# Optimization experiments

Measured on AMD Instinct MI355X. Metric: run time of the kernel, lower is better.

Reference implementation:

```python
import jax, jax.numpy as jnp
import numpy as np

RADIUS = 0.15   # group_args['radius']
NSAMPLE = 32    # group_args['nsample']
EPS = 1e-5      # BatchNorm eps


def ball_query(p, radius, k):
    # p: [B,N,3]; returns neighbor indices [B,N,K] (first K points within radius,
    # padded with the first hit -- PointNet++ ball-query semantics; self is always a hit)
    N = p.shape[1]
    d2 = jnp.sum((p[:, :, None, :] - p[:, None, :, :]) ** 2, axis=-1)  # [B,N,N]
    idx = jnp.where(d2 < radius * radius,
                    jnp.arange(N, dtype=jnp.int32)[None, None, :], N)
    idx = jnp.sort(idx, axis=-1)[..., :k]
    return jnp.where(idx == N, idx[..., :1], idx)


def conv_bn_relu(x, W, gamma, beta, mean, var):
    # 1x1 conv2d (pointwise over [N,K]) + eval-mode BN2d + ReLU
    x = jnp.einsum('oc,bcnk->bonk', W, x)
    scale = (gamma / jnp.sqrt(var + EPS))[None, :, None, None]
    shift = (beta - mean * gamma / jnp.sqrt(var + EPS))[None, :, None, None]
    return jax.nn.relu(x * scale + shift)


def setup_inputs() -> dict:
    key = jax.random.key(0)
    ks = jax.random.split(key, 4)
    B, N, C = 2, 8192, 64
    C1, C2 = 128, 128
    Cin = C + 3  # CHANNEL_MAP['dp_fj']
    return {
        'p': jax.random.uniform(ks[0], (B, N, 3), jnp.float32),
        'f': jax.random.normal(ks[1], (B, C, N), jnp.float32),
        'W1': jax.random.normal(ks[2], (C1, Cin), jnp.float32) / np.float32(np.sqrt(Cin)),
        'gamma1': jnp.ones((C1,), jnp.float32),
        'beta1': jnp.zeros((C1,), jnp.float32),
        'mean1': jnp.zeros((C1,), jnp.float32),
        'var1': jnp.ones((C1,), jnp.float32),
        'W2': jax.random.normal(ks[3], (C2, C1), jnp.float32) / np.float32(np.sqrt(C1)),
        'gamma2': jnp.ones((C2,), jnp.float32),
        'beta2': jnp.zeros((C2,), jnp.float32),
        'mean2': jnp.zeros((C2,), jnp.float32),
        'var2': jnp.ones((C2,), jnp.float32),
    }


def reference(p, f, W1, gamma1, beta1, mean1, var1, W2, gamma2, beta2, mean2, var2):
    # p: [B,N,3], f: [B,C,N]
    idx = ball_query(p, RADIUS, NSAMPLE)                                   # [B,N,K]
    gp = jnp.take_along_axis(p[:, None, :, :], idx[:, :, :, None], axis=2)  # [B,N,K,3]
    dp = jnp.transpose(gp - p[:, :, None, :], (0, 3, 1, 2))                 # [B,3,N,K]
    fj = jnp.take_along_axis(f[:, :, None, :], idx[:, None, :, :], axis=3)  # [B,C,N,K]
    x = jnp.concatenate([dp, fj], axis=1)                                   # dp_fj: [B,3+C,N,K]
    x = conv_bn_relu(x, W1, gamma1, beta1, mean1, var1)
    x = conv_bn_relu(x, W2, gamma2, beta2, mean2, var2)
    return jnp.max(x, axis=-1)                                              # [B,C2,N]
```

## Files before the change

### kernel.cpp

```cpp
#include <hip/hip_runtime.h>
#include <math.h>

#define NSAMPLE 32
constexpr int B_ = 2, N_ = 8192, C_ = 64, C1_ = 128, C2_ = 128, CIN_ = 67;
constexpr int KP = 96;
constexpr int XPAD = 104;
constexpr int HPAD = 136;
constexpr float BQ_R2 = 0.15f * 0.15f;
constexpr float EPS_ = 1e-5f;
constexpr int NCELL = 216;

typedef __attribute__((ext_vector_type(8))) short bf16x8;
typedef __attribute__((ext_vector_type(4))) short short4v;
typedef __attribute__((ext_vector_type(4))) float f32x4;
typedef unsigned long long ull;

__device__ __forceinline__ short f2bf(float x) {
    union { float f; unsigned u; } v; v.f = x;
    return (short)((v.u + 0x7FFFu + ((v.u >> 16) & 1u)) >> 16);
}
__device__ __forceinline__ int cell_id(float x, float y, float z) {
    int cx = min((int)(x * 6.0f), 5);
    int cy = min((int)(y * 6.0f), 5);
    int cz = min((int)(z * 6.0f), 5);
    return (cz * 6 + cy) * 6 + cx;
}

constexpr int TBLK = (B_ * N_) / 256;
constexpr int CBLK0 = TBLK + 1;

__global__ __launch_bounds__(256) void prep_kernel(
    const float* __restrict__ p, const float* __restrict__ f,
    short* __restrict__ fT, int* __restrict__ counts,
    const float* __restrict__ W1,
    const float* __restrict__ g1, const float* __restrict__ b1,
    const float* __restrict__ m1, const float* __restrict__ v1,
    const float* __restrict__ W2,
    const float* __restrict__ g2, const float* __restrict__ b2,
    const float* __restrict__ m2, const float* __restrict__ v2,
    short* __restrict__ W1p, short* __restrict__ W2p, float* __restrict__ bn)
{
    int blk = blockIdx.x;
    if (blk < TBLK) {
        int g = blk * 256 + threadIdx.x;
        int b = g >> 13, n = g & (N_ - 1);
        const float* fb = f + (size_t)b * C_ * N_ + n;
        short* row = fT + (size_t)g * C_;
        #pragma unroll
        for (int c0 = 0; c0 < C_; c0 += 8) {
            bf16x8 v;
            #pragma unroll
            for (int c = 0; c < 8; ++c) v[c] = f2bf(fb[(size_t)(c0 + c) * N_]);
            *(bf16x8*)&row[c0] = v;
        }
    } else if (blk == TBLK) {
        if (threadIdx.x >= 128) return;
        int t = threadIdx.x;
        short* r1 = W1p + t * KP;
        #pragma unroll
        for (int k = 0; k < 3; ++k) r1[k] = f2bf(W1[t * CIN_ + k]);
        #pragma unroll
        for (int k = 3; k < 8; ++k) r1[k] = 0;
        for (int c = 0; c < 64; ++c) r1[8 + c] = f2bf(W1[t * CIN_ + 3 + c]);
        #pragma unroll
        for (int k = 72; k < KP; ++k) r1[k] = 0;
        short* r2 = W2p + t * C1_;
        for (int c = 0; c < C1_; ++c) r2[c] = f2bf(W2[t * C1_ + c]);
        float s1 = g1[t] * rsqrtf(v1[t] + EPS_);
        bn[t] = s1;            bn[128 + t] = b1[t] - m1[t] * s1;
        float s2 = g2[t] * rsqrtf(v2[t] + EPS_);
        bn[256 + t] = s2;      bn[384 + t] = b2[t] - m2[t] * s2;
    } else {
        int g = (blk - CBLK0) * 256 + threadIdx.x;
        int b = g >> 13, n = g & (N_ - 1);
        const float* q = p + (size_t)b * N_ * 3 + 3 * n;
        int c = cell_id(q[0], q[1], q[2]);
        atomicAdd(&counts[b * 256 + c], 1);
    }
}

__global__ __launch_bounds__(128) void prefix_kernel(
    const int* __restrict__ counts, int* __restrict__ starts)
{
    int w = threadIdx.x >> 6, lane = threadIdx.x & 63;
    const int* cnt = counts + w * 256;
    int* st = starts + w * 256;
    int off = 0;
    #pragma unroll
    for (int ch = 0; ch < 4; ++ch) {
        int i = ch * 64 + lane;
        int v = (i < NCELL) ? cnt[i] : 0;
        int incl = v;
        #pragma unroll
        for (int d = 1; d < 64; d <<= 1) {
            int t = __shfl_up(incl, d, 64);
            if (lane >= d) incl += t;
        }
        if (i <= NCELL) st[i] = off + incl - v;
        off += __shfl(incl, 63, 64);
    }
}

__global__ __launch_bounds__(256) void scatter_kernel(
    const float* __restrict__ p, const int* __restrict__ starts,
    int* __restrict__ cursors, int* __restrict__ lists)
{
    int g = blockIdx.x * 256 + threadIdx.x;
    int b = g >> 13, n = g & (N_ - 1);
    const float* q = p + (size_t)b * N_ * 3 + 3 * n;
    int c = cell_id(q[0], q[1], q[2]);
    int slot = starts[b * 256 + c] + atomicAdd(&cursors[b * 256 + c], 1);
    lists[(b << 13) + slot] = n;
}

__global__ __launch_bounds__(256) void grid_query_kernel(
    const float* __restrict__ p, const int* __restrict__ starts,
    const int* __restrict__ lists, int* __restrict__ idx)
{
    __shared__ ull bitmap[4][128];
    int tid = threadIdx.x, lane = tid & 63, w = tid >> 6;
    int wid = blockIdx.x * 4 + w;
    int b = wid >> 13, n = wid & (N_ - 1);
    const float* pb = p + (size_t)b * N_ * 3;
    const int* st = starts + b * 256;
    const int* ls = lists + (b << 13);
    float qx = pb[3 * n], qy = pb[3 * n + 1], qz = pb[3 * n + 2];

    #pragma unroll
    for (int i = lane; i < 128; i += 64) bitmap[w][i] = 0;

    int cx = min((int)(qx * 6.0f), 5);
    int cy = min((int)(qy * 6.0f), 5);
    int cz = min((int)(qz * 6.0f), 5);
    int x0 = max(cx - 1, 0), x1 = min(cx + 1, 5);

    int segBase[9], segLen[9], total = 0;
    #pragma unroll
    for (int s = 0; s < 9; ++s) {
        int zz = cz - 1 + s / 3, yy = cy - 1 + s % 3;
        bool ok = (zz >= 0 && zz < 6 && yy >= 0 && yy < 6);
        int zc = min(max(zz, 0), 5), yc = min(max(yy, 0), 5);
        int row = (zc * 6 + yc) * 6;
        int s0 = st[row + x0], s1 = st[row + x1 + 1];
        segBase[s] = s0;
        segLen[s] = ok ? (s1 - s0) : 0;
        total += segLen[s];
    }

    for (int o0 = 0; o0 < total; o0 += 64) {
        int o = o0 + lane;
        if (o < total) {
            int rem = o, addr = -1;
            #pragma unroll
            for (int s = 0; s < 9; ++s) {
                if (rem >= 0 && rem < segLen[s] && addr < 0) addr = segBase[s] + rem;
                rem -= segLen[s];
            }
            int j = ls[addr];
            float dx = __fadd_rn(pb[3 * j],     -qx);
            float dy = __fadd_rn(pb[3 * j + 1], -qy);
            float dz = __fadd_rn(pb[3 * j + 2], -qz);
            float d2 = __fadd_rn(__fadd_rn(__fmul_rn(dx, dx), __fmul_rn(dy, dy)),
                                 __fmul_rn(dz, dz));
            if (d2 < BQ_R2)
                atomicOr(&bitmap[w][j >> 6], 1ull << (j & 63));
        }
    }
    __threadfence_block();

    ull w0 = bitmap[w][2 * lane], w1 = bitmap[w][2 * lane + 1];
    int c = __popcll(w0) + __popcll(w1);
    int incl = c;
    #pragma unroll
    for (int d = 1; d < 64; d <<= 1) {
        int t = __shfl_up(incl, d, 64);
        if (lane >= d) incl += t;
    }
    int pref = incl - c;
    int total_hits = __shfl(incl, 63, 64);
    int* out = idx + (size_t)wid * NSAMPLE;

    int rank = pref;
    ull ww = w0;
    int basebit = lane * 128;
    while (ww && rank < NSAMPLE) {
        int bpos = __builtin_ctzll(ww);
        out[rank] = basebit + bpos;
        ++rank; ww &= ww - 1;
    }
    ww = w1; basebit += 64;
    while (ww && rank < NSAMPLE) {
        int bpos = __builtin_ctzll(ww);
        out[rank] = basebit + bpos;
        ++rank; ww &= ww - 1;
    }

    if (total_hits < NSAMPLE) {
        ull m = __ballot(c > 0);
        int l0 = __ffsll((long long)m) - 1;
        int fb_local = w0 ? __builtin_ctzll(w0) : 64 + __builtin_ctzll(w1);
        int first = __shfl(fb_local, l0, 64) + l0 * 128;
        for (int k2 = total_hits + lane; k2 < NSAMPLE; k2 += 64) out[k2] = first;
    }
}

__global__ __launch_bounds__(256) void fused_mfma_kernel(
    const float* __restrict__ p, const int* __restrict__ idx,
    const short* __restrict__ fT, const short* __restrict__ W1p,
    const short* __restrict__ W2p, const float* __restrict__ bn,
    float* __restrict__ out)
{
    __shared__ short smem[128 * HPAD];
    __shared__ float sBN[4][128];
    __shared__ int sidx[128];

    int tid = threadIdx.x;
    int bk = blockIdx.x;
    bk = (bk & 7) * 512 + (bk >> 3);
    int b = bk >> 11;
    int n0 = (bk & 2047) * 4;
    int lane = tid & 63, w = tid >> 6;
    int lr = lane & 15, lq = lane >> 4;

    if (tid < 128) {
        sBN[0][tid] = bn[tid];       sBN[1][tid] = bn[128 + tid];
        sBN[2][tid] = bn[256 + tid]; sBN[3][tid] = bn[384 + tid];
        sidx[tid] = idx[((size_t)((b << 13) + n0)) * NSAMPLE + tid];
    }
    __syncthreads();

    const float* pb = p + (size_t)b * N_ * 3;
    #pragma unroll
    for (int pass = 0; pass < 4; ++pass) {
        int col = pass * 32 + (tid >> 3);
        int part = tid & 7;
        int j = sidx[col];
        *(bf16x8*)&smem[col * XPAD + 8 + part * 8] =
            *(const bf16x8*)&fT[((size_t)(b << 13) + j) * C_ + part * 8];
        if (part == 0) {
            int n = n0 + (col >> 5);
            bf16x8 v = {0, 0, 0, 0, 0, 0, 0, 0};
            v[0] = f2bf(__fadd_rn(pb[3 * j],     -pb[3 * n]));
            v[1] = f2bf(__fadd_rn(pb[3 * j + 1], -pb[3 * n + 1]));
            v[2] = f2bf(__fadd_rn(pb[3 * j + 2], -pb[3 * n + 2]));
            *(bf16x8*)&smem[col * XPAD] = v;
        } else if (part <= 3) {
            bf16x8 z = {0, 0, 0, 0, 0, 0, 0, 0};
            *(bf16x8*)&smem[col * XPAD + 72 + (part - 1) * 8] = z;
        }
    }
    __syncthreads();

    int wr = (w & 1) * 64;
    int wc = (w >> 1) * 64;

    f32x4 acc[4][4];
    #pragma unroll
    for (int m = 0; m < 4; ++m)
        #pragma unroll
        for (int nt = 0; nt < 4; ++nt) acc[m][nt] = (f32x4){0.f, 0.f, 0.f, 0.f};
    #pragma unroll
    for (int ks = 0; ks < 3; ++ks) {
        bf16x8 a[4];
        #pragma unroll
        for (int m = 0; m < 4; ++m)
            a[m] = *(const bf16x8*)&W1p[(wr + m * 16 + lr) * KP + ks * 32 + lq * 8];
        #pragma unroll
        for (int nt = 0; nt < 4; ++nt) {
            bf16x8 bf = *(const bf16x8*)&smem[(wc + nt * 16 + lr) * XPAD + ks * 32 + lq * 8];
            #pragma unroll
            for (int m = 0; m < 4; ++m)
                acc[m][nt] = __builtin_amdgcn_mfma_f32_16x16x32_bf16(a[m], bf, acc[m][nt], 0, 0, 0);
        }
    }
    __syncthreads();

    #pragma unroll
    for (int m = 0; m < 4; ++m) {
        int rb = wr + m * 16 + lq * 4;
        float s0 = sBN[0][rb], s1 = sBN[0][rb + 1], s2 = sBN[0][rb + 2], s3 = sBN[0][rb + 3];
        float h0 = sBN[1][rb], h1 = sBN[1][rb + 1], h2 = sBN[1][rb + 2], h3 = sBN[1][rb + 3];
        #pragma unroll
        for (int nt = 0; nt < 4; ++nt) {
            int col = wc + nt * 16 + lr;
            short4v hv;
            hv[0] = f2bf(fmaxf(fmaf(acc[m][nt][0], s0, h0), 0.f));
            hv[1] = f2bf(fmaxf(fmaf(acc[m][nt][1], s1, h1), 0.f));
            hv[2] = f2bf(fmaxf(fmaf(acc[m][nt][2], s2, h2), 0.f));
            hv[3] = f2bf(fmaxf(fmaf(acc[m][nt][3], s3, h3), 0.f));
            *(short4v*)&smem[col * HPAD + rb] = hv;
        }
    }
    __syncthreads();

    f32x4 acc2[4][4];
    #pragma unroll
    for (int m = 0; m < 4; ++m)
        #pragma unroll
        for (int nt = 0; nt < 4; ++nt) acc2[m][nt] = (f32x4){0.f, 0.f, 0.f, 0.f};
    #pragma unroll
    for (int ks = 0; ks < 4; ++ks) {
        bf16x8 a[4];
        #pragma unroll
        for (int m = 0; m < 4; ++m)
            a[m] = *(const bf16x8*)&W2p[(wr + m * 16 + lr) * C1_ + ks * 32 + lq * 8];
        #pragma unroll
        for (int nt = 0; nt < 4; ++nt) {
            bf16x8 bf = *(const bf16x8*)&smem[(wc + nt * 16 + lr) * HPAD + ks * 32 + lq * 8];
            #pragma unroll
            for (int m = 0; m < 4; ++m)
                acc2[m][nt] = __builtin_amdgcn_mfma_f32_16x16x32_bf16(a[m], bf, acc2[m][nt], 0, 0, 0);
        }
    }

    #pragma unroll
    for (int m = 0; m < 4; ++m) {
        int rb = wr + m * 16 + lq * 4;
        float s0 = sBN[2][rb], s1 = sBN[2][rb + 1], s2 = sBN[2][rb + 2], s3 = sBN[2][rb + 3];
        float h0 = sBN[3][rb], h1 = sBN[3][rb + 1], h2 = sBN[3][rb + 2], h3 = sBN[3][rb + 3];
        #pragma unroll
        for (int lp = 0; lp < 2; ++lp) {
            int n = n0 + (w >> 1) * 2 + lp;
            float v0 = fmaxf(fmaf(acc2[m][2 * lp][0], s0, h0), fmaf(acc2[m][2 * lp + 1][0], s0, h0));
            float v1 = fmaxf(fmaf(acc2[m][2 * lp][1], s1, h1), fmaf(acc2[m][2 * lp + 1][1], s1, h1));
            float v2 = fmaxf(fmaf(acc2[m][2 * lp][2], s2, h2), fmaf(acc2[m][2 * lp + 1][2], s2, h2));
            float v3 = fmaxf(fmaf(acc2[m][2 * lp][3], s3, h3), fmaf(acc2[m][2 * lp + 1][3], s3, h3));
            #pragma unroll
            for (int st = 1; st <= 8; st <<= 1) {
                v0 = fmaxf(v0, __shfl_xor(v0, st, 64));
                v1 = fmaxf(v1, __shfl_xor(v1, st, 64));
                v2 = fmaxf(v2, __shfl_xor(v2, st, 64));
                v3 = fmaxf(v3, __shfl_xor(v3, st, 64));
            }
            if (lr == 0) {
                out[((size_t)(b * C2_ + rb))     * N_ + n] = fmaxf(v0, 0.f);
                out[((size_t)(b * C2_ + rb + 1)) * N_ + n] = fmaxf(v1, 0.f);
                out[((size_t)(b * C2_ + rb + 2)) * N_ + n] = fmaxf(v2, 0.f);
                out[((size_t)(b * C2_ + rb + 3)) * N_ + n] = fmaxf(v3, 0.f);
            }
        }
    }
}

extern "C" void kernel_launch(void* const* d_in, const int* in_sizes, int n_in,
                              void* d_out, int out_size, void* d_ws, size_t ws_size,
                              hipStream_t stream) {
    const float* p   = (const float*)d_in[0];
    const float* f   = (const float*)d_in[1];
    const float* W1  = (const float*)d_in[2];
    const float* g1  = (const float*)d_in[3];
    const float* bb1 = (const float*)d_in[4];
    const float* m1  = (const float*)d_in[5];
    const float* v1  = (const float*)d_in[6];
    const float* W2  = (const float*)d_in[7];
    const float* g2  = (const float*)d_in[8];
    const float* bb2 = (const float*)d_in[9];
    const float* m2  = (const float*)d_in[10];
    const float* v2  = (const float*)d_in[11];
    float* out = (float*)d_out;

    char* ws = (char*)d_ws;
    int*   idxbuf = (int*)ws;
    short* fT  = (short*)(ws + (2 << 20));
    short* W1p = (short*)(ws + (4 << 20));
    short* W2p = (short*)(ws + (4 << 20) + 0x6000);
    float* bnv = (float*)(ws + (4 << 20) + 0xE000);
    char*  gm  = ws + (4 << 20) + 0x10000;
    int* counts  = (int*)gm;
    int* cursors = (int*)(gm + 0x800);
    int* starts  = (int*)(gm + 0x1000);
    int* lists   = (int*)(gm + 0x2000);

    hipMemsetAsync(gm, 0, 0x1000, stream);
    prep_kernel<<<CBLK0 + 64, 256, 0, stream>>>(
        p, f, fT, counts, W1, g1, bb1, m1, v1, W2, g2, bb2, m2, v2,
        W1p, W2p, bnv);
    prefix_kernel<<<1, 128, 0, stream>>>(counts, starts);
    scatter_kernel<<<64, 256, 0, stream>>>(p, starts, cursors, lists);
    grid_query_kernel<<<(B_ * N_) / 4, 256, 0, stream>>>(p, starts, lists, idxbuf);
    fused_mfma_kernel<<<(B_ * N_) / 4, 256, 0, stream>>>(
        p, idxbuf, fT, W1p, W2p, bnv, out);
}
```

Before: 217.8 us.

## Precompute per-point layer-1 feature GEMM and fuse ball query into MLP kernel

Splits the first conv so the feature part (W1·f with BN scale) is computed once per point in a separate MFMA GEMM, stored as bf16 Y. Per-neighbor work then gathers Y rows and adds the 3-channel relative-position term with scalar FMAs. This removes the K-fold redundant layer-1 GEMM. The grid ball query is also merged into the MLP kernel, which drops the global idx buffer and one launch. The cost is an extra bf16 rounding of the pre-activation Y, plus a transposed layer-2 MFMA layout.

```diff
diff --git a/kernel.cpp b/kernel.cpp
--- a/kernel.cpp
+++ b/kernel.cpp
@@ -3,12 +3,8 @@
 
 #define NSAMPLE 32
 constexpr int B_ = 2, N_ = 8192, C_ = 64, C1_ = 128, C2_ = 128, CIN_ = 67;
-constexpr int KP = 96;
-constexpr int XPAD = 104;
-constexpr int HPAD = 136;
 constexpr float BQ_R2 = 0.15f * 0.15f;
 constexpr float EPS_ = 1e-5f;
-constexpr int NCELL = 216;
 
 typedef __attribute__((ext_vector_type(8))) short bf16x8;
 typedef __attribute__((ext_vector_type(4))) short short4v;
@@ -18,6 +14,10 @@
 __device__ __forceinline__ short f2bf(float x) {
     union { float f; unsigned u; } v; v.f = x;
     return (short)((v.u + 0x7FFFu + ((v.u >> 16) & 1u)) >> 16);
+}
+__device__ __forceinline__ float bf2f(short s) {
+    union { float f; unsigned u; } v; v.u = ((unsigned)(unsigned short)s) << 16;
+    return v.f;
 }
 __device__ __forceinline__ int cell_id(float x, float y, float z) {
     int cx = min((int)(x * 6.0f), 5);
@@ -27,7 +27,6 @@
 }
 
 constexpr int TBLK = (B_ * N_) / 256;
-constexpr int CBLK0 = TBLK + 1;
 
 __global__ __launch_bounds__(256) void prep_kernel(
     const float* __restrict__ p, const float* __restrict__ f,
@@ -38,7 +37,8 @@
     const float* __restrict__ W2,
     const float* __restrict__ g2, const float* __restrict__ b2,
     const float* __restrict__ m2, const float* __restrict__ v2,
-    short* __restrict__ W1p, short* __restrict__ W2p, float* __restrict__ bn)
+    short* __restrict__ W1fp, short* __restrict__ W2p,
+    float* __restrict__ Wd, float* __restrict__ bn)
 {
     int blk = blockIdx.x;
     if (blk < TBLK) {
@@ -56,22 +56,19 @@
     } else if (blk == TBLK) {
         if (threadIdx.x >= 128) return;
         int t = threadIdx.x;
-        short* r1 = W1p + t * KP;
-        #pragma unroll
-        for (int k = 0; k < 3; ++k) r1[k] = f2bf(W1[t * CIN_ + k]);
-        #pragma unroll
-        for (int k = 3; k < 8; ++k) r1[k] = 0;
-        for (int c = 0; c < 64; ++c) r1[8 + c] = f2bf(W1[t * CIN_ + 3 + c]);
-        #pragma unroll
-        for (int k = 72; k < KP; ++k) r1[k] = 0;
+        float s1 = g1[t] * rsqrtf(v1[t] + EPS_);
+        float s2 = g2[t] * rsqrtf(v2[t] + EPS_);
+        bn[t] = s1;            bn[128 + t] = b1[t] - m1[t] * s1;
+        bn[256 + t] = s2;      bn[384 + t] = b2[t] - m2[t] * s2;
+        Wd[t]       = s1 * W1[t * CIN_ + 0];
+        Wd[128 + t] = s1 * W1[t * CIN_ + 1];
+        Wd[256 + t] = s1 * W1[t * CIN_ + 2];
+        short* r1 = W1fp + t * 64;
+        for (int c = 0; c < 64; ++c) r1[c] = f2bf(W1[t * CIN_ + 3 + c]);
         short* r2 = W2p + t * C1_;
         for (int c = 0; c < C1_; ++c) r2[c] = f2bf(W2[t * C1_ + c]);
-        float s1 = g1[t] * rsqrtf(v1[t] + EPS_);
-        bn[t] = s1;            bn[128 + t] = b1[t] - m1[t] * s1;
-        float s2 = g2[t] * rsqrtf(v2[t] + EPS_);
-        bn[256 + t] = s2;      bn[384 + t] = b2[t] - m2[t] * s2;
     } else {
-        int g = (blk - CBLK0) * 256 + threadIdx.x;
+        int g = (blk - TBLK - 1) * 256 + threadIdx.x;
         int b = g >> 13, n = g & (N_ - 1);
         const float* q = p + (size_t)b * N_ * 3 + 3 * n;
         int c = cell_id(q[0], q[1], q[2]);
@@ -89,210 +86,200 @@
     #pragma unroll
     for (int ch = 0; ch < 4; ++ch) {
         int i = ch * 64 + lane;
-        int v = (i < NCELL) ? cnt[i] : 0;
+        int v = (i < 216) ? cnt[i] : 0;
         int incl = v;
         #pragma unroll
         for (int d = 1; d < 64; d <<= 1) {
             int t = __shfl_up(incl, d, 64);
             if (lane >= d) incl += t;
         }
-        if (i <= NCELL) st[i] = off + incl - v;
+        if (i <= 216) st[i] = off + incl - v;
         off += __shfl(incl, 63, 64);
     }
 }
 
-__global__ __launch_bounds__(256) void scatter_kernel(
+__global__ __launch_bounds__(256) void scatter_ygemm_kernel(
     const float* __restrict__ p, const int* __restrict__ starts,
-    int* __restrict__ cursors, int* __restrict__ lists)
+    int* __restrict__ cursors, int* __restrict__ lists,
+    const short* __restrict__ fT, const short* __restrict__ W1fp,
+    const float* __restrict__ bn, short* __restrict__ Y)
 {
-    int g = blockIdx.x * 256 + threadIdx.x;
-    int b = g >> 13, n = g & (N_ - 1);
-    const float* q = p + (size_t)b * N_ * 3 + 3 * n;
-    int c = cell_id(q[0], q[1], q[2]);
-    int slot = starts[b * 256 + c] + atomicAdd(&cursors[b * 256 + c], 1);
-    lists[(b << 13) + slot] = n;
-}
-
-__global__ __launch_bounds__(256) void grid_query_kernel(
+    int blk = blockIdx.x;
+    if (blk < 64) {
+        int g = blk * 256 + threadIdx.x;
+        int b = g >> 13, n = g & (N_ - 1);
+        const float* q = p + (size_t)b * N_ * 3 + 3 * n;
+        int c = cell_id(q[0], q[1], q[2]);
+        int slot = starts[b * 256 + c] + atomicAdd(&cursors[b * 256 + c], 1);
+        lists[(b << 13) + slot] = n;
+        return;
+    }
+    int q = blk - 64;
+    int gs0 = q * 128;
+    int tid = threadIdx.x, lane = tid & 63, w = tid >> 6;
+    int lr = lane & 15, lq = lane >> 4;
+    int rq = (w & 1) * 64, cq = (w >> 1) * 64;
+    f32x4 acc[4][4];
+    #pragma unroll
+    for (int m = 0; m < 4; ++m)
+        #pragma unroll
+        for (int nt = 0; nt < 4; ++nt) acc[m][nt] = (f32x4){0.f, 0.f, 0.f, 0.f};
+    #pragma unroll
+    for (int ks = 0; ks < 2; ++ks) {
+        bf16x8 a[4];
+        #pragma unroll
+        for (int m = 0; m < 4; ++m)
+            a[m] = *(const bf16x8*)&W1fp[(rq + m * 16 + lr) * 64 + ks * 32 + lq * 8];
+        #pragma unroll
+        for (int nt = 0; nt < 4; ++nt) {
+            bf16x8 bfr = *(const bf16x8*)&fT[((size_t)(gs0 + cq + nt * 16 + lr)) * 64 + ks * 32 + lq * 8];
+            #pragma unroll
+            for (int m = 0; m < 4; ++m)
+                acc[m][nt] = __builtin_amdgcn_mfma_f32_16x16x32_bf16(a[m], bfr, acc[m][nt], 0, 0, 0);
+        }
+    }
+    #pragma unroll
+    for (int m = 0; m < 4; ++m) {
+        int rb = rq + m * 16 + lq * 4;
+        f32x4 sc = *(const f32x4*)&bn[rb];
+        f32x4 sh = *(const f32x4*)&bn[128 + rb];
+        #pragma unroll
+        for (int nt = 0; nt < 4; ++nt) {
+            int gs = gs0 + cq + nt * 16 + lr;
+            short4v yv;
+            yv[0] = f2bf(fmaf(acc[m][nt][0], sc[0], sh[0]));
+            yv[1] = f2bf(fmaf(acc[m][nt][1], sc[1], sh[1]));
+            yv[2] = f2bf(fmaf(acc[m][nt][2], sc[2], sh[2]));
+            yv[3] = f2bf(fmaf(acc[m][nt][3], sc[3], sh[3]));
+            *(short4v*)&Y[(size_t)gs * 128 + rb] = yv;
+        }
+    }
+}
+
+__global__ __launch_bounds__(256) void fused_kernel(
     const float* __restrict__ p, const int* __restrict__ starts,
-    const int* __restrict__ lists, int* __restrict__ idx)
+    const int* __restrict__ lists, const short* __restrict__ Y,
+    const short* __restrict__ W2p, const float* __restrict__ Wd,
+    const float* __restrict__ bn, float* __restrict__ out)
 {
     __shared__ ull bitmap[4][128];
-    int tid = threadIdx.x, lane = tid & 63, w = tid >> 6;
-    int wid = blockIdx.x * 4 + w;
-    int b = wid >> 13, n = wid & (N_ - 1);
+    __shared__ int sidx[4][NSAMPLE];
+    __shared__ short HT[16 * 128 * 8];
+
+    int tid = threadIdx.x;
+    int bk = blockIdx.x;
+    bk = (bk & 7) * 512 + (bk >> 3);
+    int b = bk >> 11, n0 = (bk & 2047) * 4;
+    int lane = tid & 63, w = tid >> 6;
+    int lr = lane & 15, lq = lane >> 4;
     const float* pb = p + (size_t)b * N_ * 3;
     const int* st = starts + b * 256;
     const int* ls = lists + (b << 13);
-    float qx = pb[3 * n], qy = pb[3 * n + 1], qz = pb[3 * n + 2];
-
-    #pragma unroll
-    for (int i = lane; i < 128; i += 64) bitmap[w][i] = 0;
-
+
+    int nq = n0 + w;
+    float qx = pb[3 * nq], qy = pb[3 * nq + 1], qz = pb[3 * nq + 2];
+    *(f32x4*)&bitmap[w][2 * lane] = (f32x4){0.f, 0.f, 0.f, 0.f};
     int cx = min((int)(qx * 6.0f), 5);
     int cy = min((int)(qy * 6.0f), 5);
     int cz = min((int)(qz * 6.0f), 5);
     int x0 = max(cx - 1, 0), x1 = min(cx + 1, 5);
-
-    int segBase[9], segLen[9], total = 0;
-    #pragma unroll
-    for (int s = 0; s < 9; ++s) {
-        int zz = cz - 1 + s / 3, yy = cy - 1 + s % 3;
-        bool ok = (zz >= 0 && zz < 6 && yy >= 0 && yy < 6);
-        int zc = min(max(zz, 0), 5), yc = min(max(yy, 0), 5);
-        int row = (zc * 6 + yc) * 6;
-        int s0 = st[row + x0], s1 = st[row + x1 + 1];
-        segBase[s] = s0;
-        segLen[s] = ok ? (s1 - s0) : 0;
-        total += segLen[s];
-    }
-
-    for (int o0 = 0; o0 < total; o0 += 64) {
-        int o = o0 + lane;
-        if (o < total) {
-            int rem = o, addr = -1;
-            #pragma unroll
-            for (int s = 0; s < 9; ++s) {
-                if (rem >= 0 && rem < segLen[s] && addr < 0) addr = segBase[s] + rem;
-                rem -= segLen[s];
+    for (int s9 = 0; s9 < 9; ++s9) {
+        int zz = cz - 1 + s9 / 3, yy = cy - 1 + s9 % 3;
+        if (zz < 0 || zz > 5 || yy < 0 || yy > 5) continue;
+        int row = (zz * 6 + yy) * 6;
+        int s0 = st[row + x0];
+        int len = st[row + x1 + 1] - s0;
+        for (int o0 = 0; o0 < len; o0 += 64) {
+            int o = o0 + lane;
+            if (o < len) {
+                int j = ls[s0 + o];
+                float dx = __fadd_rn(pb[3 * j],     -qx);
+                float dy = __fadd_rn(pb[3 * j + 1], -qy);
+                float dz = __fadd_rn(pb[3 * j + 2], -qz);
+                float d2 = __fadd_rn(__fadd_rn(__fmul_rn(dx, dx), __fmul_rn(dy, dy)),
+                                     __fmul_rn(dz, dz));
+                if (d2 < BQ_R2)
+                    atomicOr(&bitmap[w][j >> 6], 1ull << (j & 63));
             }
-            int j = ls[addr];
-            float dx = __fadd_rn(pb[3 * j],     -qx);
-            float dy = __fadd_rn(pb[3 * j + 1], -qy);
-            float dz = __fadd_rn(pb[3 * j + 2], -qz);
-            float d2 = __fadd_rn(__fadd_rn(__fmul_rn(dx, dx), __fmul_rn(dy, dy)),
-                                 __fmul_rn(dz, dz));
-            if (d2 < BQ_R2)
-                atomicOr(&bitmap[w][j >> 6], 1ull << (j & 63));
-        }
-    }
-    __threadfence_block();
-
-    ull w0 = bitmap[w][2 * lane], w1 = bitmap[w][2 * lane + 1];
-    int c = __popcll(w0) + __popcll(w1);
-    int incl = c;
-    #pragma unroll
-    for (int d = 1; d < 64; d <<= 1) {
-        int t = __shfl_up(incl, d, 64);
-        if (lane >= d) incl += t;
-    }
-    int pref = incl - c;
-    int total_hits = __shfl(incl, 63, 64);
-    int* out = idx + (size_t)wid * NSAMPLE;
-
-    int rank = pref;
-    ull ww = w0;
-    int basebit = lane * 128;
-    while (ww && rank < NSAMPLE) {
-        int bpos = __builtin_ctzll(ww);
-        out[rank] = basebit + bpos;
-        ++rank; ww &= ww - 1;
-    }
-    ww = w1; basebit += 64;
-    while (ww && rank < NSAMPLE) {
-        int bpos = __builtin_ctzll(ww);
-        out[rank] = basebit + bpos;
-        ++rank; ww &= ww - 1;
-    }
-
-    if (total_hits < NSAMPLE) {
-        ull m = __ballot(c > 0);
-        int l0 = __ffsll((long long)m) - 1;
-        int fb_local = w0 ? __builtin_ctzll(w0) : 64 + __builtin_ctzll(w1);
-        int first = __shfl(fb_local, l0, 64) + l0 * 128;
-        for (int k2 = total_hits + lane; k2 < NSAMPLE; k2 += 64) out[k2] = first;
-    }
-}
-
-__global__ __launch_bounds__(256) void fused_mfma_kernel(
-    const float* __restrict__ p, const int* __restrict__ idx,
-    const short* __restrict__ fT, const short* __restrict__ W1p,
-    const short* __restrict__ W2p, const float* __restrict__ bn,
-    float* __restrict__ out)
-{
-    __shared__ short smem[128 * HPAD];
-    __shared__ float sBN[4][128];
-    __shared__ int sidx[128];
-
-    int tid = threadIdx.x;
-    int bk = blockIdx.x;
-    bk = (bk & 7) * 512 + (bk >> 3);
-    int b = bk >> 11;
-    int n0 = (bk & 2047) * 4;
-    int lane = tid & 63, w = tid >> 6;
-    int lr = lane & 15, lq = lane >> 4;
-
-    if (tid < 128) {
-        sBN[0][tid] = bn[tid];       sBN[1][tid] = bn[128 + tid];
-        sBN[2][tid] = bn[256 + tid]; sBN[3][tid] = bn[384 + tid];
-        sidx[tid] = idx[((size_t)((b << 13) + n0)) * NSAMPLE + tid];
+        }
     }
     __syncthreads();
 
-    const float* pb = p + (size_t)b * N_ * 3;
-    #pragma unroll
-    for (int pass = 0; pass < 4; ++pass) {
-        int col = pass * 32 + (tid >> 3);
-        int part = tid & 7;
-        int j = sidx[col];
-        *(bf16x8*)&smem[col * XPAD + 8 + part * 8] =
-            *(const bf16x8*)&fT[((size_t)(b << 13) + j) * C_ + part * 8];
-        if (part == 0) {
-            int n = n0 + (col >> 5);
-            bf16x8 v = {0, 0, 0, 0, 0, 0, 0, 0};
-            v[0] = f2bf(__fadd_rn(pb[3 * j],     -pb[3 * n]));
-            v[1] = f2bf(__fadd_rn(pb[3 * j + 1], -pb[3 * n + 1]));
-            v[2] = f2bf(__fadd_rn(pb[3 * j + 2], -pb[3 * n + 2]));
-            *(bf16x8*)&smem[col * XPAD] = v;
-        } else if (part <= 3) {
-            bf16x8 z = {0, 0, 0, 0, 0, 0, 0, 0};
-            *(bf16x8*)&smem[col * XPAD + 72 + (part - 1) * 8] = z;
+    {
+        ull w0 = bitmap[w][2 * lane], w1 = bitmap[w][2 * lane + 1];
+        int c = __popcll(w0) + __popcll(w1);
+        int incl = c;
+        #pragma unroll
+        for (int d = 1; d < 64; d <<= 1) {
+            int t = __shfl_up(incl, d, 64);
+            if (lane >= d) incl += t;
+        }
+        int pref = incl - c;
+        int total_hits = __shfl(incl, 63, 64);
+        int rank = pref;
+        ull ww = w0;
+        int basebit = lane * 128;
+        while (ww && rank < NSAMPLE) {
+            sidx[w][rank] = basebit + __builtin_ctzll(ww);
+            ++rank; ww &= ww - 1;
+        }
+        ww = w1; basebit += 64;
+        while (ww && rank < NSAMPLE) {
+            sidx[w][rank] = basebit + __builtin_ctzll(ww);
+            ++rank; ww &= ww - 1;
+        }
+        if (total_hits < NSAMPLE) {
+            ull m = __ballot(c > 0);
+            int l0 = __ffsll((long long)m) - 1;
+            int fb_local = w0 ? __builtin_ctzll(w0) : 64 + __builtin_ctzll(w1);
+            int first = __shfl(fb_local, l0, 64) + l0 * 128;
+            for (int k2 = total_hits + lane; k2 < NSAMPLE; k2 += 64) sidx[w][k2] = first;
         }
     }
     __syncthreads();
 
-    int wr = (w & 1) * 64;
+    {
+        int sl = lane & 31, g = lane >> 5;
+        int S = w * 32 + sl;
+        int j = sidx[w][sl];
+        float ax = __fadd_rn(pb[3 * j],     -qx);
+        float ay = __fadd_rn(pb[3 * j + 1], -qy);
+        float az = __fadd_rn(pb[3 * j + 2], -qz);
+        const short* yrow = Y + ((size_t)((b << 13) + j)) * 128;
+        #pragma unroll
+        for (int pp = 0; pp < 4; ++pp) {
+            int ch0 = (pp * 2 + g) * 16;
+            bf16x8 ylo = *(const bf16x8*)&yrow[ch0];
+            bf16x8 yhi = *(const bf16x8*)&yrow[ch0 + 8];
+            union { f32x4 v[4]; float s[16]; } wxa, wya, wza;
+            #pragma unroll
+            for (int k = 0; k < 4; ++k) {
+                wxa.v[k] = *(const f32x4*)&Wd[ch0 + 4 * k];
+                wya.v[k] = *(const f32x4*)&Wd[128 + ch0 + 4 * k];
+                wza.v[k] = *(const f32x4*)&Wd[256 + ch0 + 4 * k];
+            }
+            bf16x8 lo, hi;
+            #pragma unroll
+            for (int i = 0; i < 8; ++i) {
+                float yv = bf2f(ylo[i]);
+                float h = fmaf(az, wza.s[i], fmaf(ay, wya.s[i], fmaf(ax, wxa.s[i], yv)));
+                lo[i] = f2bf(fmaxf(h, 0.f));
+            }
+            #pragma unroll
+            for (int i = 0; i < 8; ++i) {
+                float yv = bf2f(yhi[i]);
+                float h = fmaf(az, wza.s[8 + i], fmaf(ay, wya.s[8 + i], fmaf(ax, wxa.s[8 + i], yv)));
+                hi[i] = f2bf(fmaxf(h, 0.f));
+            }
+            int slot = ch0 >> 3;
+            *(bf16x8*)&HT[(slot * 128 + S) * 8]       = lo;
+            *(bf16x8*)&HT[((slot + 1) * 128 + S) * 8] = hi;
+        }
+    }
+    __syncthreads();
+
+    int sb = (w & 1) * 64;
     int wc = (w >> 1) * 64;
-
-    f32x4 acc[4][4];
-    #pragma unroll
-    for (int m = 0; m < 4; ++m)
-        #pragma unroll
-        for (int nt = 0; nt < 4; ++nt) acc[m][nt] = (f32x4){0.f, 0.f, 0.f, 0.f};
-    #pragma unroll
-    for (int ks = 0; ks < 3; ++ks) {
-        bf16x8 a[4];
-        #pragma unroll
-        for (int m = 0; m < 4; ++m)
-            a[m] = *(const bf16x8*)&W1p[(wr + m * 16 + lr) * KP + ks * 32 + lq * 8];
-        #pragma unroll
-        for (int nt = 0; nt < 4; ++nt) {
-            bf16x8 bf = *(const bf16x8*)&smem[(wc + nt * 16 + lr) * XPAD + ks * 32 + lq * 8];
-            #pragma unroll
-            for (int m = 0; m < 4; ++m)
-                acc[m][nt] = __builtin_amdgcn_mfma_f32_16x16x32_bf16(a[m], bf, acc[m][nt], 0, 0, 0);
-        }
-    }
-    __syncthreads();
-
-    #pragma unroll
-    for (int m = 0; m < 4; ++m) {
-        int rb = wr + m * 16 + lq * 4;
-        float s0 = sBN[0][rb], s1 = sBN[0][rb + 1], s2 = sBN[0][rb + 2], s3 = sBN[0][rb + 3];
-        float h0 = sBN[1][rb], h1 = sBN[1][rb + 1], h2 = sBN[1][rb + 2], h3 = sBN[1][rb + 3];
-        #pragma unroll
-        for (int nt = 0; nt < 4; ++nt) {
-            int col = wc + nt * 16 + lr;
-            short4v hv;
-            hv[0] = f2bf(fmaxf(fmaf(acc[m][nt][0], s0, h0), 0.f));
-            hv[1] = f2bf(fmaxf(fmaf(acc[m][nt][1], s1, h1), 0.f));
-            hv[2] = f2bf(fmaxf(fmaf(acc[m][nt][2], s2, h2), 0.f));
-            hv[3] = f2bf(fmaxf(fmaf(acc[m][nt][3], s3, h3), 0.f));
-            *(short4v*)&smem[col * HPAD + rb] = hv;
-        }
-    }
-    __syncthreads();
-
     f32x4 acc2[4][4];
     #pragma unroll
     for (int m = 0; m < 4; ++m)
@@ -303,41 +290,35 @@
         bf16x8 a[4];
         #pragma unroll
         for (int m = 0; m < 4; ++m)
-            a[m] = *(const bf16x8*)&W2p[(wr + m * 16 + lr) * C1_ + ks * 32 + lq * 8];
+            a[m] = *(const bf16x8*)&HT[((ks * 4 + lq) * 128 + sb + m * 16 + lr) * 8];
         #pragma unroll
         for (int nt = 0; nt < 4; ++nt) {
-            bf16x8 bf = *(const bf16x8*)&smem[(wc + nt * 16 + lr) * HPAD + ks * 32 + lq * 8];
+            bf16x8 bw = *(const bf16x8*)&W2p[(wc + nt * 16 + lr) * C1_ + ks * 32 + lq * 8];
             #pragma unroll
             for (int m = 0; m < 4; ++m)
-                acc2[m][nt] = __builtin_amdgcn_mfma_f32_16x16x32_bf16(a[m], bf, acc2[m][nt], 0, 0, 0);
-        }
-    }
-
-    #pragma unroll
-    for (int m = 0; m < 4; ++m) {
-        int rb = wr + m * 16 + lq * 4;
-        float s0 = sBN[2][rb], s1 = sBN[2][rb + 1], s2 = sBN[2][rb + 2], s3 = sBN[2][rb + 3];
-        float h0 = sBN[3][rb], h1 = sBN[3][rb + 1], h2 = sBN[3][rb + 2], h3 = sBN[3][rb + 3];
-        #pragma unroll
-        for (int lp = 0; lp < 2; ++lp) {
-            int n = n0 + (w >> 1) * 2 + lp;
-            float v0 = fmaxf(fmaf(acc2[m][2 * lp][0], s0, h0), fmaf(acc2[m][2 * lp + 1][0], s0, h0));
-            float v1 = fmaxf(fmaf(acc2[m][2 * lp][1], s1, h1), fmaf(acc2[m][2 * lp + 1][1], s1, h1));
-            float v2 = fmaxf(fmaf(acc2[m][2 * lp][2], s2, h2), fmaf(acc2[m][2 * lp + 1][2], s2, h2));
-            float v3 = fmaxf(fmaf(acc2[m][2 * lp][3], s3, h3), fmaf(acc2[m][2 * lp + 1][3], s3, h3));
-            #pragma unroll
-            for (int st = 1; st <= 8; st <<= 1) {
-                v0 = fmaxf(v0, __shfl_xor(v0, st, 64));
-                v1 = fmaxf(v1, __shfl_xor(v1, st, 64));
-                v2 = fmaxf(v2, __shfl_xor(v2, st, 64));
-                v3 = fmaxf(v3, __shfl_xor(v3, st, 64));
-            }
-            if (lr == 0) {
-                out[((size_t)(b * C2_ + rb))     * N_ + n] = fmaxf(v0, 0.f);
-                out[((size_t)(b * C2_ + rb + 1)) * N_ + n] = fmaxf(v1, 0.f);
-                out[((size_t)(b * C2_ + rb + 2)) * N_ + n] = fmaxf(v2, 0.f);
-                out[((size_t)(b * C2_ + rb + 3)) * N_ + n] = fmaxf(v3, 0.f);
-            }
+                acc2[m][nt] = __builtin_amdgcn_mfma_f32_16x16x32_bf16(a[m], bw, acc2[m][nt], 0, 0, 0);
+        }
+    }
+
+    #pragma unroll
+    for (int nt = 0; nt < 4; ++nt) {
+        int ch = wc + nt * 16 + lr;
+        float sc = bn[256 + ch], sh = bn[384 + ch];
+        #pragma unroll
+        for (int pt = 0; pt < 2; ++pt) {
+            int m0 = pt * 2;
+            float v =          fmaf(acc2[m0][nt][0],     sc, sh);
+            v = fmaxf(v, fmaf(acc2[m0][nt][1],     sc, sh));
+            v = fmaxf(v, fmaf(acc2[m0][nt][2],     sc, sh));
+            v = fmaxf(v, fmaf(acc2[m0][nt][3],     sc, sh));
+            v = fmaxf(v, fmaf(acc2[m0 + 1][nt][0], sc, sh));
+            v = fmaxf(v, fmaf(acc2[m0 + 1][nt][1], sc, sh));
+            v = fmaxf(v, fmaf(acc2[m0 + 1][nt][2], sc, sh));
+            v = fmaxf(v, fmaf(acc2[m0 + 1][nt][3], sc, sh));
+            v = fmaxf(v, __shfl_xor(v, 16, 64));
+            v = fmaxf(v, __shfl_xor(v, 32, 64));
+            if (lq == 0)
+                out[((size_t)(b * C2_ + ch)) * N_ + n0 + (w & 1) * 2 + pt] = fmaxf(v, 0.f);
         }
     }
 }
@@ -360,24 +341,26 @@
     float* out = (float*)d_out;
 
     char* ws = (char*)d_ws;
-    int*   idxbuf = (int*)ws;
-    short* fT  = (short*)(ws + (2 << 20));
-    short* W1p = (short*)(ws + (4 << 20));
-    short* W2p = (short*)(ws + (4 << 20) + 0x6000);
-    float* bnv = (float*)(ws + (4 << 20) + 0xE000);
-    char*  gm  = ws + (4 << 20) + 0x10000;
+    short* fT   = (short*)ws;
+    short* Y    = (short*)(ws + (2 << 20));
+    char*  wb   = ws + (6 << 20);
+    short* W1fp = (short*)wb;
+    short* W2p  = (short*)(wb + 0x4000);
+    float* Wd   = (float*)(wb + 0xC000);
+    float* bnv  = (float*)(wb + 0xD000);
+    char*  gm   = wb + 0xE000;
     int* counts  = (int*)gm;
     int* cursors = (int*)(gm + 0x800);
     int* starts  = (int*)(gm + 0x1000);
     int* lists   = (int*)(gm + 0x2000);
 
     hipMemsetAsync(gm, 0, 0x1000, stream);
-    prep_kernel<<<CBLK0 + 64, 256, 0, stream>>>(
+    prep_kernel<<<TBLK + 1 + 64, 256, 0, stream>>>(
         p, f, fT, counts, W1, g1, bb1, m1, v1, W2, g2, bb2, m2, v2,
-        W1p, W2p, bnv);
+        W1fp, W2p, Wd, bnv);
     prefix_kernel<<<1, 128, 0, stream>>>(counts, starts);
-    scatter_kernel<<<64, 256, 0, stream>>>(p, starts, cursors, lists);
-    grid_query_kernel<<<(B_ * N_) / 4, 256, 0, stream>>>(p, starts, lists, idxbuf);
-    fused_mfma_kernel<<<(B_ * N_) / 4, 256, 0, stream>>>(
-        p, idxbuf, fT, W1p, W2p, bnv, out);
-}
+    scatter_ygemm_kernel<<<64 + 128, 256, 0, stream>>>(
+        p, starts, cursors, lists, fT, W1fp, bnv, Y);
+    fused_kernel<<<(B_ * N_) / 4, 256, 0, stream>>>(
+        p, starts, lists, Y, W2p, Wd, bnv, out);
+}
```

Result: slower. 248.7 us (+14.2%).

## Fuse grid build into prep kernel and transpose second GEMM layout

Applied to the files above, without the earlier changes.

The separate count, prefix and scatter kernels and the memset are folded into the prep kernel. One block per batch builds the cell histogram, the prefix sum and the scatter using shared-memory atomics, which removes three launches. The second GEMM in the fused kernel now takes the hidden activations from LDS as the A operand, stored in a k-blocked layout, and reads W2 from global as B. The max over neighbours then runs mostly in registers with two cross-lane shuffles. The per-batch scatter runs serially in just two blocks, and list order inside each cell is no longer deterministic.

```diff
diff --git a/kernel.cpp b/kernel.cpp
--- a/kernel.cpp
+++ b/kernel.cpp
@@ -5,10 +5,8 @@
 constexpr int B_ = 2, N_ = 8192, C_ = 64, C1_ = 128, C2_ = 128, CIN_ = 67;
 constexpr int KP = 96;
 constexpr int XPAD = 104;
-constexpr int HPAD = 136;
 constexpr float BQ_R2 = 0.15f * 0.15f;
 constexpr float EPS_ = 1e-5f;
-constexpr int NCELL = 216;
 
 typedef __attribute__((ext_vector_type(8))) short bf16x8;
 typedef __attribute__((ext_vector_type(4))) short short4v;
@@ -27,22 +25,23 @@
 }
 
 constexpr int TBLK = (B_ * N_) / 256;
-constexpr int CBLK0 = TBLK + 1;
-
-__global__ __launch_bounds__(256) void prep_kernel(
+
+__global__ __launch_bounds__(256) void prep_all_kernel(
     const float* __restrict__ p, const float* __restrict__ f,
-    short* __restrict__ fT, int* __restrict__ counts,
+    short* __restrict__ fT,
     const float* __restrict__ W1,
     const float* __restrict__ g1, const float* __restrict__ b1,
     const float* __restrict__ m1, const float* __restrict__ v1,
     const float* __restrict__ W2,
     const float* __restrict__ g2, const float* __restrict__ b2,
     const float* __restrict__ m2, const float* __restrict__ v2,
-    short* __restrict__ W1p, short* __restrict__ W2p, float* __restrict__ bn)
+    short* __restrict__ W1p, short* __restrict__ W2p, float* __restrict__ bn,
+    int* __restrict__ starts, int* __restrict__ lists)
 {
     int blk = blockIdx.x;
+    int tid = threadIdx.x;
     if (blk < TBLK) {
-        int g = blk * 256 + threadIdx.x;
+        int g = blk * 256 + tid;
         int b = g >> 13, n = g & (N_ - 1);
         const float* fb = f + (size_t)b * C_ * N_ + n;
         short* row = fT + (size_t)g * C_;
@@ -54,8 +53,8 @@
             *(bf16x8*)&row[c0] = v;
         }
     } else if (blk == TBLK) {
-        if (threadIdx.x >= 128) return;
-        int t = threadIdx.x;
+        if (tid >= 128) return;
+        int t = tid;
         short* r1 = W1p + t * KP;
         #pragma unroll
         for (int k = 0; k < 3; ++k) r1[k] = f2bf(W1[t * CIN_ + k]);
@@ -71,46 +70,44 @@
         float s2 = g2[t] * rsqrtf(v2[t] + EPS_);
         bn[256 + t] = s2;      bn[384 + t] = b2[t] - m2[t] * s2;
     } else {
-        int g = (blk - CBLK0) * 256 + threadIdx.x;
-        int b = g >> 13, n = g & (N_ - 1);
-        const float* q = p + (size_t)b * N_ * 3 + 3 * n;
-        int c = cell_id(q[0], q[1], q[2]);
-        atomicAdd(&counts[b * 256 + c], 1);
-    }
-}
-
-__global__ __launch_bounds__(128) void prefix_kernel(
-    const int* __restrict__ counts, int* __restrict__ starts)
-{
-    int w = threadIdx.x >> 6, lane = threadIdx.x & 63;
-    const int* cnt = counts + w * 256;
-    int* st = starts + w * 256;
-    int off = 0;
-    #pragma unroll
-    for (int ch = 0; ch < 4; ++ch) {
-        int i = ch * 64 + lane;
-        int v = (i < NCELL) ? cnt[i] : 0;
-        int incl = v;
-        #pragma unroll
-        for (int d = 1; d < 64; d <<= 1) {
-            int t = __shfl_up(incl, d, 64);
-            if (lane >= d) incl += t;
-        }
-        if (i <= NCELL) st[i] = off + incl - v;
-        off += __shfl(incl, 63, 64);
-    }
-}
-
-__global__ __launch_bounds__(256) void scatter_kernel(
-    const float* __restrict__ p, const int* __restrict__ starts,
-    int* __restrict__ cursors, int* __restrict__ lists)
-{
-    int g = blockIdx.x * 256 + threadIdx.x;
-    int b = g >> 13, n = g & (N_ - 1);
-    const float* q = p + (size_t)b * N_ * 3 + 3 * n;
-    int c = cell_id(q[0], q[1], q[2]);
-    int slot = starts[b * 256 + c] + atomicAdd(&cursors[b * 256 + c], 1);
-    lists[(b << 13) + slot] = n;
+        __shared__ int scnt[256];
+        __shared__ int scur[256];
+        int bb = blk - TBLK - 1;
+        const float* pbB = p + (size_t)bb * N_ * 3;
+        for (int i = tid; i < 256; i += 256) scnt[i] = 0;
+        __syncthreads();
+        for (int n = tid; n < N_; n += 256) {
+            int c = cell_id(pbB[3 * n], pbB[3 * n + 1], pbB[3 * n + 2]);
+            atomicAdd(&scnt[c], 1);
+        }
+        __syncthreads();
+        if (tid < 64) {
+            int off = 0;
+            #pragma unroll
+            for (int ch = 0; ch < 4; ++ch) {
+                int i = ch * 64 + tid;
+                int v = (i < 216) ? scnt[i] : 0;
+                int incl = v;
+                #pragma unroll
+                for (int d = 1; d < 64; d <<= 1) {
+                    int t2 = __shfl_up(incl, d, 64);
+                    if (tid >= d) incl += t2;
+                }
+                if (i <= 216) {
+                    int ex = off + incl - v;
+                    starts[bb * 256 + i] = ex;
+                    if (i < 216) scur[i] = ex;
+                }
+                off += __shfl(incl, 63, 64);
+            }
+        }
+        __syncthreads();
+        for (int n = tid; n < N_; n += 256) {
+            int c = cell_id(pbB[3 * n], pbB[3 * n + 1], pbB[3 * n + 2]);
+            int slot = atomicAdd(&scur[c], 1);
+            lists[(bb << 13) + slot] = n;
+        }
+    }
 }
 
 __global__ __launch_bounds__(256) void grid_query_kernel(
@@ -184,14 +181,12 @@
     ull ww = w0;
     int basebit = lane * 128;
     while (ww && rank < NSAMPLE) {
-        int bpos = __builtin_ctzll(ww);
-        out[rank] = basebit + bpos;
+        out[rank] = basebit + __builtin_ctzll(ww);
         ++rank; ww &= ww - 1;
     }
     ww = w1; basebit += 64;
     while (ww && rank < NSAMPLE) {
-        int bpos = __builtin_ctzll(ww);
-        out[rank] = basebit + bpos;
+        out[rank] = basebit + __builtin_ctzll(ww);
         ++rank; ww &= ww - 1;
     }
 
@@ -210,7 +205,7 @@
     const short* __restrict__ W2p, const float* __restrict__ bn,
     float* __restrict__ out)
 {
-    __shared__ short smem[128 * HPAD];
+    __shared__ short smem[16 * 128 * 8];
     __shared__ float sBN[4][128];
     __shared__ int sidx[128];
 
@@ -288,11 +283,13 @@
             hv[1] = f2bf(fmaxf(fmaf(acc[m][nt][1], s1, h1), 0.f));
             hv[2] = f2bf(fmaxf(fmaf(acc[m][nt][2], s2, h2), 0.f));
             hv[3] = f2bf(fmaxf(fmaf(acc[m][nt][3], s3, h3), 0.f));
-            *(short4v*)&smem[col * HPAD + rb] = hv;
+            *(short4v*)&smem[((rb >> 3) * 128 + col) * 8 + (rb & 7)] = hv;
         }
     }
     __syncthreads();
 
+    int sb = (w & 1) * 64;
+    int wc2 = (w >> 1) * 64;
     f32x4 acc2[4][4];
     #pragma unroll
     for (int m = 0; m < 4; ++m)
@@ -303,41 +300,35 @@
         bf16x8 a[4];
         #pragma unroll
         for (int m = 0; m < 4; ++m)
-            a[m] = *(const bf16x8*)&W2p[(wr + m * 16 + lr) * C1_ + ks * 32 + lq * 8];
+            a[m] = *(const bf16x8*)&smem[((ks * 4 + lq) * 128 + sb + m * 16 + lr) * 8];
         #pragma unroll
         for (int nt = 0; nt < 4; ++nt) {
-            bf16x8 bf = *(const bf16x8*)&smem[(wc + nt * 16 + lr) * HPAD + ks * 32 + lq * 8];
+            bf16x8 bw = *(const bf16x8*)&W2p[(wc2 + nt * 16 + lr) * C1_ + ks * 32 + lq * 8];
             #pragma unroll
             for (int m = 0; m < 4; ++m)
-                acc2[m][nt] = __builtin_amdgcn_mfma_f32_16x16x32_bf16(a[m], bf, acc2[m][nt], 0, 0, 0);
-        }
-    }
-
-    #pragma unroll
-    for (int m = 0; m < 4; ++m) {
-        int rb = wr + m * 16 + lq * 4;
-        float s0 = sBN[2][rb], s1 = sBN[2][rb + 1], s2 = sBN[2][rb + 2], s3 = sBN[2][rb + 3];
-        float h0 = sBN[3][rb], h1 = sBN[3][rb + 1], h2 = sBN[3][rb + 2], h3 = sBN[3][rb + 3];
-        #pragma unroll
-        for (int lp = 0; lp < 2; ++lp) {
-            int n = n0 + (w >> 1) * 2 + lp;
-            float v0 = fmaxf(fmaf(acc2[m][2 * lp][0], s0, h0), fmaf(acc2[m][2 * lp + 1][0], s0, h0));
-            float v1 = fmaxf(fmaf(acc2[m][2 * lp][1], s1, h1), fmaf(acc2[m][2 * lp + 1][1], s1, h1));
-            float v2 = fmaxf(fmaf(acc2[m][2 * lp][2], s2, h2), fmaf(acc2[m][2 * lp + 1][2], s2, h2));
-            float v3 = fmaxf(fmaf(acc2[m][2 * lp][3], s3, h3), fmaf(acc2[m][2 * lp + 1][3], s3, h3));
-            #pragma unroll
-            for (int st = 1; st <= 8; st <<= 1) {
-                v0 = fmaxf(v0, __shfl_xor(v0, st, 64));
-                v1 = fmaxf(v1, __shfl_xor(v1, st, 64));
-                v2 = fmaxf(v2, __shfl_xor(v2, st, 64));
-                v3 = fmaxf(v3, __shfl_xor(v3, st, 64));
-            }
-            if (lr == 0) {
-                out[((size_t)(b * C2_ + rb))     * N_ + n] = fmaxf(v0, 0.f);
-                out[((size_t)(b * C2_ + rb + 1)) * N_ + n] = fmaxf(v1, 0.f);
-                out[((size_t)(b * C2_ + rb + 2)) * N_ + n] = fmaxf(v2, 0.f);
-                out[((size_t)(b * C2_ + rb + 3)) * N_ + n] = fmaxf(v3, 0.f);
-            }
+                acc2[m][nt] = __builtin_amdgcn_mfma_f32_16x16x32_bf16(a[m], bw, acc2[m][nt], 0, 0, 0);
+        }
+    }
+
+    #pragma unroll
+    for (int nt = 0; nt < 4; ++nt) {
+        int ch = wc2 + nt * 16 + lr;
+        float sc = sBN[2][ch], sh = sBN[3][ch];
+        #pragma unroll
+        for (int pt = 0; pt < 2; ++pt) {
+            int m0 = pt * 2;
+            float v =    fmaf(acc2[m0][nt][0],     sc, sh);
+            v = fmaxf(v, fmaf(acc2[m0][nt][1],     sc, sh));
+            v = fmaxf(v, fmaf(acc2[m0][nt][2],     sc, sh));
+            v = fmaxf(v, fmaf(acc2[m0][nt][3],     sc, sh));
+            v = fmaxf(v, fmaf(acc2[m0 + 1][nt][0], sc, sh));
+            v = fmaxf(v, fmaf(acc2[m0 + 1][nt][1], sc, sh));
+            v = fmaxf(v, fmaf(acc2[m0 + 1][nt][2], sc, sh));
+            v = fmaxf(v, fmaf(acc2[m0 + 1][nt][3], sc, sh));
+            v = fmaxf(v, __shfl_xor(v, 16, 64));
+            v = fmaxf(v, __shfl_xor(v, 32, 64));
+            if (lq == 0)
+                out[((size_t)(b * C2_ + ch)) * N_ + n0 + (w & 1) * 2 + pt] = fmaxf(v, 0.f);
         }
     }
 }
@@ -366,17 +357,12 @@
     short* W2p = (short*)(ws + (4 << 20) + 0x6000);
     float* bnv = (float*)(ws + (4 << 20) + 0xE000);
     char*  gm  = ws + (4 << 20) + 0x10000;
-    int* counts  = (int*)gm;
-    int* cursors = (int*)(gm + 0x800);
-    int* starts  = (int*)(gm + 0x1000);
-    int* lists   = (int*)(gm + 0x2000);
-
-    hipMemsetAsync(gm, 0, 0x1000, stream);
-    prep_kernel<<<CBLK0 + 64, 256, 0, stream>>>(
-        p, f, fT, counts, W1, g1, bb1, m1, v1, W2, g2, bb2, m2, v2,
-        W1p, W2p, bnv);
-    prefix_kernel<<<1, 128, 0, stream>>>(counts, starts);
-    scatter_kernel<<<64, 256, 0, stream>>>(p, starts, cursors, lists);
+    int* starts  = (int*)gm;
+    int* lists   = (int*)(gm + 0x1000);
+
+    prep_all_kernel<<<TBLK + 3, 256, 0, stream>>>(
+        p, f, fT, W1, g1, bb1, m1, v1, W2, g2, bb2, m2, v2,
+        W1p, W2p, bnv, starts, lists);
     grid_query_kernel<<<(B_ * N_) / 4, 256, 0, stream>>>(p, starts, lists, idxbuf);
     fused_mfma_kernel<<<(B_ * N_) / 4, 256, 0, stream>>>(
         p, idxbuf, fT, W1p, W2p, bnv, out);
```

Measured after the change: 199.5 us. 1.09x faster.
